# Kernel optimization log

Measured on AMD Instinct MI355X. Metric: run time of the kernel, lower is better.

The kernel has to match this reference:

```python
import jax, jax.numpy as jnp
import numpy as np

# Conv2dfft forward (no spectral compression: preserve_energy=None, index_back=None, out_size=None)
# Implements cross-correlation (DL convolution) via rfft2 / irfft2, matching the torch module's
# padding and output-size logic:
#   out_H = H - HH + 1 + 2*pad ; init_fft = H + 2*pad + max(out_H, HH) - 1

PAD = 1  # padding from init_kwargs


def setup_inputs() -> dict:
    key = jax.random.key(0)
    k1, k2, k3 = jax.random.split(key, 3)
    x = jax.random.normal(k1, (32, 128, 32, 32), dtype=jnp.float32)
    w = jax.random.normal(k2, (128, 128, 3, 3), dtype=jnp.float32) * 0.1
    b = jax.random.normal(k3, (128,), dtype=jnp.float32)
    return {"x": x, "w": w, "b": b}


def reference(x, w, b):
    N, C, H, W = x.shape
    F, _, HH, WW = w.shape
    out_H = H - HH + 1 + 2 * PAD
    out_W = W - WW + 1 + 2 * PAD
    init_fft_H = H + 2 * PAD + max(out_H, HH) - 1  # 65
    init_fft_W = W + 2 * PAD + max(out_W, WW) - 1  # 65

    # pad input: explicit conv padding + zero-pad up to FFT grid
    fft_pad_H = init_fft_H - 2 * PAD - H
    fft_pad_W = init_fft_W - 2 * PAD - W
    px = jnp.pad(x, ((0, 0), (0, 0), (PAD, PAD + fft_pad_H), (PAD, PAD + fft_pad_W)))
    pw = jnp.pad(w, ((0, 0), (0, 0), (0, init_fft_H - HH), (0, init_fft_W - WW)))

    xfft = jnp.fft.rfft2(px)                     # [N,C,65,33] complex64
    yfft = jnp.fft.rfft2(pw)                     # [F,C,65,33] complex64

    # cross-correlation: multiply by conj(filter fft), accumulate over input channels
    prod = jnp.einsum('nchw,fchw->nfhw', xfft, jnp.conj(yfft))
    full = jnp.fft.irfft2(prod, s=(init_fft_H, init_fft_W))  # [N,F,65,65]
    out = full[:, :, :out_H, :out_W] + b[None, :, None, None]
    return out
```

## Files before the change

kernel.cpp:

```cpp
#include <hip/hip_runtime.h>


typedef __attribute__((ext_vector_type(8))) short bf16x8;
typedef __attribute__((ext_vector_type(4))) float f32x4;

#define N_IMG 32
#define C_IN  128
#define F_OUT 128
#define HW    32
#define HPAD  34

__device__ __forceinline__ unsigned short f2bf(float f) {
    union { float f; unsigned u; } v; v.f = f;
    unsigned r = v.u + 0x7fffu + ((v.u >> 16) & 1u);
    return (unsigned short)(r >> 16);
}

__global__ __launch_bounds__(256) void pack_x_kernel(const float* __restrict__ x,
                                                     unsigned short* __restrict__ xp) {
    __shared__ unsigned short tile[C_IN * HPAD];
    const int n   = blockIdx.x / HPAD;
    const int hp  = blockIdx.x - n * HPAD;
    const int tid = threadIdx.x;
    const unsigned base_out = (unsigned)(n * HPAD + hp) * (HPAD * C_IN);
    if (hp >= 1 && hp <= 32) {
        const int h = hp - 1;
        #pragma unroll
        for (int i = 0; i < 16; ++i) {
            int idx = tid + i * 256;
            int c = idx >> 5, w = idx & 31;
            tile[c * HPAD + (w + 1)] = f2bf(x[((n * C_IN + c) * HW + h) * HW + w]);
        }
        if (tid < C_IN) { tile[tid * HPAD] = 0; tile[tid * HPAD + 33] = 0; }
        __syncthreads();
        #pragma unroll
        for (int i = 0; i < 17; ++i) {
            int idx = tid + i * 256;
            int wp = idx >> 7, c = idx & 127;
            xp[base_out + (unsigned)idx] = tile[c * HPAD + wp];
        }
    } else {
        #pragma unroll
        for (int i = 0; i < 17; ++i) {
            int idx = tid + i * 256;
            xp[base_out + (unsigned)idx] = 0;
        }
    }
}

__global__ __launch_bounds__(256) void pack_w_kernel(const float* __restrict__ w,
                                                     unsigned short* __restrict__ wpk) {
    int idx = blockIdx.x * 256 + threadIdx.x;
    int ci = idx & 31;
    int f  = (idx >> 5) & 127;
    int cc = (idx >> 12) & 3;
    int t  = idx >> 14;
    int c  = cc * 32 + ci;
    wpk[idx] = f2bf(w[(f * C_IN + c) * 9 + t]);
}

__global__ __launch_bounds__(256, 1) void conv_gemm_kernel(
    const unsigned short* __restrict__ xp,
    const unsigned short* __restrict__ wpk,
    const float* __restrict__ bias,
    float* __restrict__ out)
{
    __shared__ alignas(16) unsigned short lds_x[10 * HPAD * 32];
    __shared__ alignas(16) unsigned short lds_a[5 * 64 * 32];

    const int tid  = threadIdx.x;
    const int lane = tid & 63;
    const int wave = tid >> 6;
    const int qk   = lane >> 4;
    const int l15  = lane & 15;

    const int f0 = (blockIdx.x & 1) * 64;
    const int pb = blockIdx.x >> 1;
    const int n  = pb >> 2;
    const int h0 = (pb & 3) * 8;

    f32x4 acc[4][4];
    #pragma unroll
    for (int mi = 0; mi < 4; ++mi)
        #pragma unroll
        for (int ni = 0; ni < 4; ++ni)
            acc[mi][ni] = (f32x4){0.f, 0.f, 0.f, 0.f};

    int b_base[4];
    #pragma unroll
    for (int ni = 0; ni < 4; ++ni) {
        int p = wave * 64 + ni * 16 + l15;
        b_base[ni] = ((p >> 5) * HPAD + (p & 31)) * 32 + qk * 8;
    }
    const int a_off = l15 * 32 + qk * 8;

    const unsigned short* xsrc0 = xp + (unsigned)((n * HPAD + h0) * HPAD) * C_IN;

    for (int cc = 0; cc < 4; ++cc) {
        __syncthreads();
        #pragma unroll
        for (int i = 0; i < 6; ++i) {
            int idx = tid + i * 256;
            if (idx < 1360) {
                unsigned g = (unsigned)idx >> 2;
                int dh = (int)(g / 34u);
                int wv = (int)(g - (unsigned)dh * 34u);
                int ci0 = (idx & 3) * 8;
                const unsigned short* src = xsrc0 + (dh * HPAD + wv) * C_IN + cc * 32 + ci0;
                __builtin_amdgcn_global_load_lds(
                    (const __attribute__((address_space(1))) void*)src,
                    (__attribute__((address_space(3))) void*)(&lds_x[idx * 8]),
                    16, 0, 0);
            }
        }
        #pragma unroll
        for (int half = 0; half < 2; ++half) {
            const int t0 = half ? 5 : 0;
            const int ntaps = half ? 4 : 5;
            if (half) __syncthreads();
            #pragma unroll
            for (int i = 0; i < 5; ++i) {
                int idx = tid + i * 256;
                if (idx < ntaps * 256) {
                    int tl = idx >> 8;
                    int rem = idx & 255;
                    const unsigned short* src =
                        wpk + (unsigned)((((t0 + tl) * 4 + cc) * 128) + f0 + (rem >> 2)) * 32
                            + (rem & 3) * 8;
                    __builtin_amdgcn_global_load_lds(
                        (const __attribute__((address_space(1))) void*)src,
                        (__attribute__((address_space(3))) void*)(&lds_a[idx * 8]),
                        16, 0, 0);
                }
            }
            __syncthreads();
            #pragma unroll
            for (int tl = 0; tl < 5; ++tl) {
                if (tl < ntaps) {
                    const int t = t0 + tl;
                    const int r = t / 3, s = t - r * 3;
                    const int tap_off = (r * HPAD + s) * 32;
                    bf16x8 af[4], bfr[4];
                    #pragma unroll
                    for (int mi = 0; mi < 4; ++mi)
                        af[mi] = *(const bf16x8*)&lds_a[tl * 2048 + mi * 512 + a_off];
                    #pragma unroll
                    for (int ni = 0; ni < 4; ++ni)
                        bfr[ni] = *(const bf16x8*)&lds_x[b_base[ni] + tap_off];
                    #pragma unroll
                    for (int mi = 0; mi < 4; ++mi)
                        #pragma unroll
                        for (int ni = 0; ni < 4; ++ni)
                            acc[mi][ni] = __builtin_amdgcn_mfma_f32_16x16x32_bf16(
                                af[mi], bfr[ni], acc[mi][ni], 0, 0, 0);
                }
            }
        }
    }

    #pragma unroll
    for (int mi = 0; mi < 4; ++mi) {
        const int f_base = f0 + mi * 16 + qk * 4;
        float bv[4];
        #pragma unroll
        for (int r = 0; r < 4; ++r) bv[r] = bias[f_base + r];
        #pragma unroll
        for (int ni = 0; ni < 4; ++ni) {
            int p = wave * 64 + ni * 16 + l15;
            int h = h0 + (p >> 5), w2 = p & 31;
            #pragma unroll
            for (int r = 0; r < 4; ++r) {
                out[((unsigned)(n * F_OUT + f_base + r) * HW + h) * HW + w2] =
                    acc[mi][ni][r] + bv[r];
            }
        }
    }
}

extern "C" void kernel_launch(void* const* d_in, const int* in_sizes, int n_in,
                              void* d_out, int out_size, void* d_ws, size_t ws_size,
                              hipStream_t stream) {
    const float* x = (const float*)d_in[0];
    const float* w = (const float*)d_in[1];
    const float* b = (const float*)d_in[2];
    float* out = (float*)d_out;

    unsigned short* xp  = (unsigned short*)d_ws;
    unsigned short* wpk = xp + (size_t)N_IMG * HPAD * HPAD * C_IN;

    pack_x_kernel<<<N_IMG * HPAD, 256, 0, stream>>>(x, xp);
    pack_w_kernel<<<576, 256, 0, stream>>>(w, wpk);
    conv_gemm_kernel<<<256, 256, 0, stream>>>(xp, wpk, b, out);
}
```

Before: 92.97 us.

## Halve conv GEMM tile height, double grid, swizzle LDS, load all taps at once

The implicit-GEMM conv kernel now covers a 4-row band per block instead of 8, so the grid doubles to 512 blocks and launch bounds allow two blocks per CU. The weight pack is reordered so each channel chunk's nine taps sit contiguously, and all nine taps load into LDS in one stage, removing the mid-chunk barrier. LDS rows are XOR-swizzled to reduce bank conflicts. The trade-off is more halo reloading per output and a larger weight LDS footprint, in exchange for better occupancy and fewer syncs.

```diff
diff --git a/kernel.cpp b/kernel.cpp
--- a/kernel.cpp
+++ b/kernel.cpp
@@ -53,20 +53,20 @@
     int idx = blockIdx.x * 256 + threadIdx.x;
     int ci = idx & 31;
     int f  = (idx >> 5) & 127;
-    int cc = (idx >> 12) & 3;
-    int t  = idx >> 14;
-    int c  = cc * 32 + ci;
-    wpk[idx] = f2bf(w[(f * C_IN + c) * 9 + t]);
+    int u  = idx >> 12;
+    int cc = u / 9;
+    int t  = u - cc * 9;
+    wpk[idx] = f2bf(w[(f * C_IN + cc * 32 + ci) * 9 + t]);
 }
 
-__global__ __launch_bounds__(256, 1) void conv_gemm_kernel(
+__global__ __launch_bounds__(256, 2) void conv_gemm_kernel(
     const unsigned short* __restrict__ xp,
     const unsigned short* __restrict__ wpk,
     const float* __restrict__ bias,
     float* __restrict__ out)
 {
-    __shared__ alignas(16) unsigned short lds_x[10 * HPAD * 32];
-    __shared__ alignas(16) unsigned short lds_a[5 * 64 * 32];
+    __shared__ alignas(16) unsigned short lds_x[1024 * 8];
+    __shared__ alignas(16) unsigned short lds_a[2304 * 8];
 
     const int tid  = threadIdx.x;
     const int lane = tid & 63;
@@ -74,104 +74,90 @@
     const int qk   = lane >> 4;
     const int l15  = lane & 15;
 
-    const int f0 = (blockIdx.x & 1) * 64;
-    const int pb = blockIdx.x >> 1;
-    const int n  = pb >> 2;
-    const int h0 = (pb & 3) * 8;
+    const int fh   = blockIdx.x & 1;
+    const int band = (blockIdx.x >> 1) & 7;
+    const int n    = blockIdx.x >> 4;
+    const int f0   = fh * 64;
+    const int h0   = band * 4;
 
-    f32x4 acc[4][4];
+    f32x4 acc[4][2];
     #pragma unroll
     for (int mi = 0; mi < 4; ++mi)
         #pragma unroll
-        for (int ni = 0; ni < 4; ++ni)
+        for (int ni = 0; ni < 2; ++ni)
             acc[mi][ni] = (f32x4){0.f, 0.f, 0.f, 0.f};
 
-    int b_base[4];
+    const int a_lane = l15 * 32 + (((qk ^ (l15 >> 1)) & 3) << 3);
+    int brow0[2];
     #pragma unroll
-    for (int ni = 0; ni < 4; ++ni) {
-        int p = wave * 64 + ni * 16 + l15;
-        b_base[ni] = ((p >> 5) * HPAD + (p & 31)) * 32 + qk * 8;
-    }
-    const int a_off = l15 * 32 + qk * 8;
+    for (int ni = 0; ni < 2; ++ni)
+        brow0[ni] = wave * HPAD + ni * 16 + l15;
 
     const unsigned short* xsrc0 = xp + (unsigned)((n * HPAD + h0) * HPAD) * C_IN;
+    const unsigned short* wbase = wpk + f0 * 32;
 
     for (int cc = 0; cc < 4; ++cc) {
         __syncthreads();
         #pragma unroll
-        for (int i = 0; i < 6; ++i) {
-            int idx = tid + i * 256;
-            if (idx < 1360) {
-                unsigned g = (unsigned)idx >> 2;
-                int dh = (int)(g / 34u);
-                int wv = (int)(g - (unsigned)dh * 34u);
-                int ci0 = (idx & 3) * 8;
-                const unsigned short* src = xsrc0 + (dh * HPAD + wv) * C_IN + cc * 32 + ci0;
-                __builtin_amdgcn_global_load_lds(
-                    (const __attribute__((address_space(1))) void*)src,
-                    (__attribute__((address_space(3))) void*)(&lds_x[idx * 8]),
-                    16, 0, 0);
+        for (int i = 0; i < 4; ++i) {
+            int p = tid + i * 256;
+            int row = p >> 2;  if (row > 203) row = 203;
+            int lc = (p ^ (row >> 1)) & 3;
+            const unsigned short* src = xsrc0 + row * C_IN + cc * 32 + lc * 8;
+            __builtin_amdgcn_global_load_lds(
+                (const __attribute__((address_space(1))) void*)src,
+                (__attribute__((address_space(3))) void*)(&lds_x[p * 8]),
+                16, 0, 0);
+        }
+        const unsigned short* wsrc = wbase + cc * 36864;
+        #pragma unroll
+        for (int j = 0; j < 9; ++j) {
+            int q = tid + j * 256;
+            int row = q >> 2;
+            int lc = (q ^ (row >> 1)) & 3;
+            const unsigned short* src = wsrc + ((row >> 6) * 4096) + ((row & 63) * 32) + lc * 8;
+            __builtin_amdgcn_global_load_lds(
+                (const __attribute__((address_space(1))) void*)src,
+                (__attribute__((address_space(3))) void*)(&lds_a[q * 8]),
+                16, 0, 0);
+        }
+        __syncthreads();
+        #pragma unroll
+        for (int tap = 0; tap < 9; ++tap) {
+            const int r = tap / 3, s = tap - 3 * (tap / 3);
+            bf16x8 af[4], bf[2];
+            #pragma unroll
+            for (int mi = 0; mi < 4; ++mi)
+                af[mi] = *(const bf16x8*)&lds_a[tap * 2048 + mi * 512 + a_lane];
+            #pragma unroll
+            for (int ni = 0; ni < 2; ++ni) {
+                int row = brow0[ni] + (r * HPAD + s);
+                int el  = (row << 5) + (((qk ^ (row >> 1)) & 3) << 3);
+                bf[ni] = *(const bf16x8*)&lds_x[el];
             }
-        }
-        #pragma unroll
-        for (int half = 0; half < 2; ++half) {
-            const int t0 = half ? 5 : 0;
-            const int ntaps = half ? 4 : 5;
-            if (half) __syncthreads();
             #pragma unroll
-            for (int i = 0; i < 5; ++i) {
-                int idx = tid + i * 256;
-                if (idx < ntaps * 256) {
-                    int tl = idx >> 8;
-                    int rem = idx & 255;
-                    const unsigned short* src =
-                        wpk + (unsigned)((((t0 + tl) * 4 + cc) * 128) + f0 + (rem >> 2)) * 32
-                            + (rem & 3) * 8;
-                    __builtin_amdgcn_global_load_lds(
-                        (const __attribute__((address_space(1))) void*)src,
-                        (__attribute__((address_space(3))) void*)(&lds_a[idx * 8]),
-                        16, 0, 0);
-                }
-            }
-            __syncthreads();
-            #pragma unroll
-            for (int tl = 0; tl < 5; ++tl) {
-                if (tl < ntaps) {
-                    const int t = t0 + tl;
-                    const int r = t / 3, s = t - r * 3;
-                    const int tap_off = (r * HPAD + s) * 32;
-                    bf16x8 af[4], bfr[4];
-                    #pragma unroll
-                    for (int mi = 0; mi < 4; ++mi)
-                        af[mi] = *(const bf16x8*)&lds_a[tl * 2048 + mi * 512 + a_off];
-                    #pragma unroll
-                    for (int ni = 0; ni < 4; ++ni)
-                        bfr[ni] = *(const bf16x8*)&lds_x[b_base[ni] + tap_off];
-                    #pragma unroll
-                    for (int mi = 0; mi < 4; ++mi)
-                        #pragma unroll
-                        for (int ni = 0; ni < 4; ++ni)
-                            acc[mi][ni] = __builtin_amdgcn_mfma_f32_16x16x32_bf16(
-                                af[mi], bfr[ni], acc[mi][ni], 0, 0, 0);
-                }
-            }
+            for (int mi = 0; mi < 4; ++mi)
+                #pragma unroll
+                for (int ni = 0; ni < 2; ++ni)
+                    acc[mi][ni] = __builtin_amdgcn_mfma_f32_16x16x32_bf16(
+                        af[mi], bf[ni], acc[mi][ni], 0, 0, 0);
         }
     }
 
+    const int h = h0 + wave;
     #pragma unroll
     for (int mi = 0; mi < 4; ++mi) {
         const int f_base = f0 + mi * 16 + qk * 4;
         float bv[4];
         #pragma unroll
-        for (int r = 0; r < 4; ++r) bv[r] = bias[f_base + r];
+        for (int r2 = 0; r2 < 4; ++r2) bv[r2] = bias[f_base + r2];
         #pragma unroll
-        for (int ni = 0; ni < 4; ++ni) {
-            int p = wave * 64 + ni * 16 + l15;
-            int h = h0 + (p >> 5), w2 = p & 31;
+        for (int ni = 0; ni < 2; ++ni) {
+            const int w2 = ni * 16 + l15;
             #pragma unroll
-            for (int r = 0; r < 4; ++r) {
-                out[((unsigned)(n * F_OUT + f_base + r) * HW + h) * HW + w2] =
-                    acc[mi][ni][r] + bv[r];
+            for (int r2 = 0; r2 < 4; ++r2) {
+                out[((unsigned)(n * F_OUT + f_base + r2) * HW + h) * HW + w2] =
+                    acc[mi][ni][r2] + bv[r2];
             }
         }
     }
@@ -190,5 +176,5 @@
 
     pack_x_kernel<<<N_IMG * HPAD, 256, 0, stream>>>(x, xp);
     pack_w_kernel<<<576, 256, 0, stream>>>(w, wpk);
-    conv_gemm_kernel<<<256, 256, 0, stream>>>(xp, wpk, b, out);
+    conv_gemm_kernel<<<512, 256, 0, stream>>>(xp, wpk, b, out);
 }
```

After: 90.64 us. -2.5%, faster.
